# Optimization experiments

Hardware: AMD Instinct MI355X
Metric: run time of the kernel (lower is better)

## Reference

```python
import jax, jax.numpy as jnp
import numpy as np

D_MODEL = 1024
N_HEAD = 16
HEAD_DIM = D_MODEL // N_HEAD
BATCH = 2
SEQ = 2048


def setup_inputs() -> dict:
    key = jax.random.key(0)
    ks = jax.random.split(key, 5)
    std = np.sqrt(2.0 / (D_MODEL + D_MODEL)).astype(np.float32)
    return {
        "in_features": jax.random.normal(ks[0], (BATCH, SEQ, D_MODEL), dtype=jnp.float32),
        "Wq": jax.random.normal(ks[1], (D_MODEL, D_MODEL), dtype=jnp.float32) * std,
        "Wk": jax.random.normal(ks[2], (D_MODEL, D_MODEL), dtype=jnp.float32) * std,
        "Wv": jax.random.normal(ks[3], (D_MODEL, D_MODEL), dtype=jnp.float32) * std,
        "Wo": jax.random.normal(ks[4], (D_MODEL, D_MODEL), dtype=jnp.float32) * std,
    }


def reference(in_features, Wq, Wk, Wv, Wo):
    B, S, _ = in_features.shape
    # projections: x @ W (custom Linear stores weight as [in, out], no bias)
    q = (in_features @ Wq).reshape(B, S, N_HEAD, HEAD_DIM).transpose(0, 2, 1, 3)  # [B,H,S,Dh]
    k = (in_features @ Wk).reshape(B, S, N_HEAD, HEAD_DIM).transpose(0, 2, 1, 3)
    v = (in_features @ Wv).reshape(B, S, N_HEAD, HEAD_DIM).transpose(0, 2, 1, 3)
    scale = HEAD_DIM ** (-0.5)
    scores = jnp.einsum("bhqd,bhkd->bhqk", q, k) * scale  # [B,H,S,S]
    causal = jnp.tril(jnp.ones((S, S), dtype=bool))
    scores = jnp.where(causal, scores, -jnp.inf)
    attn = jax.nn.softmax(scores, axis=-1)
    ctx = jnp.einsum("bhqk,bhkd->bhqd", attn, v)  # [B,H,S,Dh]
    ctx = ctx.transpose(0, 2, 1, 3).reshape(B, S, D_MODEL)
    return ctx @ Wo
```

## Files before the change

kernel.cpp:

```cpp
#include <hip/hip_runtime.h>
#include <hip/hip_bf16.h>

#define DM 1024
#define NH 16
#define HD 64
#define B_ 2
#define S_ 2048
#define M_ (B_*S_)

typedef __attribute__((ext_vector_type(8))) short bf16x8;
typedef __attribute__((ext_vector_type(4))) float f32x4;
typedef __attribute__((ext_vector_type(4))) unsigned uint32x4;
typedef __attribute__((ext_vector_type(2))) unsigned uint32x2;

__device__ __forceinline__ float bf2f(ushort u) {
  union { unsigned u32; float f; } c; c.u32 = ((unsigned)u) << 16; return c.f;
}
__device__ __forceinline__ ushort f2bf(float f) {
  union { float f; unsigned u32; } c; c.f = f;
  unsigned u = c.u32;
  unsigned r = (u + 0x7fffu + ((u >> 16) & 1u)) >> 16;
  return (ushort)r;
}
__device__ __forceinline__ unsigned fbits(float f) {
  union { float f; unsigned u; } c; c.f = f; return c.u;
}

__device__ __forceinline__ void async16(const ushort* g, ushort* l) {
  __builtin_amdgcn_global_load_lds((const __attribute__((address_space(1))) void*)g,
                                   (__attribute__((address_space(3))) void*)l, 16, 0, 0);
}

__device__ __forceinline__ void pswap32(unsigned& a, unsigned& b) {
  uint32x2 r = __builtin_amdgcn_permlane32_swap(a, b, false, false);
  a = r[0]; b = r[1];
}
__device__ __forceinline__ void pswap16(unsigned& a, unsigned& b) {
  uint32x2 r = __builtin_amdgcn_permlane16_swap(a, b, false, false);
  a = r[0]; b = r[1];
}

__global__ void cvt_prep(const float* __restrict__ x, const float* __restrict__ W0,
                         const float* __restrict__ W1, const float* __restrict__ W2,
                         const float* __restrict__ W3, ushort* __restrict__ wt,
                         ushort* __restrict__ xb) {
  __shared__ float tile[64][65];
  int z = blockIdx.z;
  int tx = threadIdx.x, ty = threadIdx.y;
  if (z == 4) {
    int tid = ty * 64 + tx;
    size_t base4 = ((size_t)blockIdx.y * 16 + blockIdx.x) * 4096;
    const float4* xv = (const float4*)x;
    ushort4* ov = (ushort4*)xb;
    #pragma unroll
    for (int k = 0; k < 16; ++k) {
      float4 v = xv[base4 + k * 256 + tid];
      ushort4 o;
      o.x = f2bf(v.x); o.y = f2bf(v.y); o.z = f2bf(v.z); o.w = f2bf(v.w);
      ov[base4 + k * 256 + tid] = o;
    }
    return;
  }
  const float* W = (z == 0) ? W0 : (z == 1) ? W1 : (z == 2) ? W2 : W3;
  ushort* Wt = wt + (size_t)z * (DM * DM);
  int c0 = blockIdx.x * 64, r0 = blockIdx.y * 64;
  #pragma unroll
  for (int i = ty; i < 64; i += 4) tile[i][tx] = W[(size_t)(r0 + i) * DM + c0 + tx];
  __syncthreads();
  #pragma unroll
  for (int i = ty; i < 64; i += 4) Wt[(size_t)(c0 + i) * DM + r0 + tx] = f2bf(tile[tx][i]);
}

template <int MODE, int BN>
__device__ __forceinline__ void gemm_body(const ushort* __restrict__ A,
                                          const ushort* __restrict__ Bt,
                                          ushort* __restrict__ Cb,
                                          float* __restrict__ Cf,
                                          ushort* As, ushort* Bs, ushort* Ts) {
  const int K = DM;
  constexpr int CN = BN / 32;
  int m0 = blockIdx.y * 128;
  int n0 = blockIdx.x * BN;
  int t = threadIdx.x;
  int lane = t & 63, wave = t >> 6;
  int wm = (wave >> 1) * 64, wn = (wave & 1) * (BN / 2);
  int lrow = lane & 15, quad = lane >> 4;

  int Ra = wave * 32;
  int Rb = wave * (BN / 4);
  int srow = lane >> 2, scol = (lane & 3) * 8;

  f32x4 acc[4][CN];
  #pragma unroll
  for (int r = 0; r < 4; ++r)
    #pragma unroll
    for (int c = 0; c < CN; ++c) acc[r][c] = (f32x4){0.f, 0.f, 0.f, 0.f};

  for (int k0 = 0; k0 < K; k0 += 32) {
    const ushort* ga = A + (size_t)(m0 + Ra + srow) * K + k0 + scol;
    const ushort* gb = Bt + (size_t)(n0 + Rb + srow) * K + k0 + scol;
    async16(ga,          As + Ra * 32);
    async16(ga + 16 * K, As + (Ra + 16) * 32);
    async16(gb,          Bs + Rb * 32);
    if (BN == 128) async16(gb + 16 * K, Bs + (Rb + 16) * 32);
    __syncthreads();

    bf16x8 af[4], bfr[CN];
    #pragma unroll
    for (int r = 0; r < 4; ++r)
      af[r] = *(const bf16x8*)(As + (wm + r * 16 + lrow) * 32 + quad * 8);
    #pragma unroll
    for (int c = 0; c < CN; ++c)
      bfr[c] = *(const bf16x8*)(Bs + (wn + c * 16 + lrow) * 32 + quad * 8);
    #pragma unroll
    for (int r = 0; r < 4; ++r)
      #pragma unroll
      for (int c = 0; c < CN; ++c)
        acc[r][c] = __builtin_amdgcn_mfma_f32_16x16x32_bf16(af[r], bfr[c], acc[r][c], 0, 0, 0);
    __syncthreads();
  }

  if constexpr (MODE == 2) {
    int bb = m0 >> 11;
    int s0base = m0 & 2047;
    #pragma unroll
    for (int H = 0; H < 2; ++H) {
      __syncthreads();
      if ((wave >> 1) == H) {
        #pragma unroll
        for (int r = 0; r < 4; ++r)
          #pragma unroll
          for (int c = 0; c < 4; ++c) {
            uint2 pk;
            pk.x = (unsigned)f2bf(acc[r][c][0]) | ((unsigned)f2bf(acc[r][c][1]) << 16);
            pk.y = (unsigned)f2bf(acc[r][c][2]) | ((unsigned)f2bf(acc[r][c][3]) << 16);
            *(uint2*)(Ts + (wn + c * 16 + lrow) * 72 + r * 16 + quad * 4) = pk;
          }
      }
      __syncthreads();
      #pragma unroll
      for (int i = 0; i < 4; ++i) {
        int id = t + i * 256;
        int nn = id >> 3, col = (id & 7) * 8;
        uint4 v = *(const uint4*)(Ts + nn * 72 + col);
        int h2 = (n0 >> 6) + (nn >> 6), d2 = nn & 63;
        size_t dst = (((size_t)(bb * NH + h2)) * HD + d2) * (size_t)S_ + s0base + H * 64 + col;
        *(uint4*)(Cb + dst) = v;
      }
    }
  } else {
    #pragma unroll
    for (int r = 0; r < 4; ++r) {
      #pragma unroll
      for (int c = 0; c < CN; ++c) {
        #pragma unroll
        for (int e = 0; e < 4; ++e) {
          int m = m0 + wm + r * 16 + quad * 4 + e;
          int n = n0 + wn + c * 16 + lrow;
          if (MODE == 0) {
            Cf[(size_t)m * DM + n] = acc[r][c][e];
          } else {
            int b = m >> 11, s = m & 2047, h = n >> 6, d = n & 63;
            Cb[(((size_t)(b * NH + h)) * S_ + s) * HD + d] = f2bf(acc[r][c][e]);
          }
        }
      }
    }
  }
}

__global__ __launch_bounds__(256, 3) void gemm_qkv(const ushort* __restrict__ A,
                                                   const ushort* __restrict__ wt,
                                                   ushort* __restrict__ qkv) {
  __shared__ __align__(16) ushort smem[9216];
  ushort* As = smem;
  ushort* Bs = smem + 4096;
  ushort* Ts = smem;
  int z = blockIdx.z;
  if (z < 2)
    gemm_body<1, 128>(A, wt + (size_t)z * (DM * DM), qkv + (size_t)z * ((size_t)M_ * DM),
                      nullptr, As, Bs, Ts);
  else
    gemm_body<2, 128>(A, wt + (size_t)2 * (DM * DM), qkv + (size_t)2 * ((size_t)M_ * DM),
                      nullptr, As, Bs, Ts);
}

__global__ __launch_bounds__(256, 3) void gemm_out(const ushort* __restrict__ A,
                                                   const ushort* __restrict__ wt,
                                                   float* __restrict__ C) {
  __shared__ __align__(16) ushort As[128 * 32];
  __shared__ __align__(16) ushort Bs[64 * 32];
  gemm_body<0, 64>(A, wt, nullptr, C, As, Bs, nullptr);
}

#define EXPC 0.18033688011f

struct AttnState {
  f32x4 o[4];
  float l;
};

template <bool MASKED>
__device__ __forceinline__ void attn_tile_compute(
    int q0, int kt, bf16x8 qf0, bf16x8 qf1,
    const bf16x8 kf0[4], const bf16x8 kf1[4],
    const bf16x8 vf0[4], const bf16x8 vf1[4],
    AttnState& st, int lrow, int quad) {
  f32x4 s[4];
  __builtin_amdgcn_s_setprio(1);
  #pragma unroll
  for (int c = 0; c < 4; ++c) {
    f32x4 z = (f32x4){0.f, 0.f, 0.f, 0.f};
    z = __builtin_amdgcn_mfma_f32_16x16x32_bf16(kf0[c], qf0, z, 0, 0, 0);
    z = __builtin_amdgcn_mfma_f32_16x16x32_bf16(kf1[c], qf1, z, 0, 0, 0);
    s[c] = z;
  }
  __builtin_amdgcn_s_setprio(0);
  int q = q0 + lrow;
  unsigned w0[4], w1[4];
  #pragma unroll
  for (int c = 0; c < 4; ++c) {
    float pv[4];
    #pragma unroll
    for (int e = 0; e < 4; ++e) {
      float v = __builtin_amdgcn_exp2f(s[c][e] * EXPC);
      if (MASKED) {
        int key = kt + c * 16 + quad * 4 + e;
        v = (key <= q) ? v : 0.f;
      }
      pv[e] = v;
      st.l += v;
    }
    w0[c] = __builtin_amdgcn_perm(fbits(pv[1]), fbits(pv[0]), 0x07060302u);
    w1[c] = __builtin_amdgcn_perm(fbits(pv[3]), fbits(pv[2]), 0x07060302u);
  }

  unsigned a0 = w0[0], b0 = w0[1]; pswap32(a0, b0); pswap16(a0, b0);
  unsigned a1 = w1[0], b1 = w1[1]; pswap32(a1, b1); pswap16(a1, b1);
  unsigned c0 = w0[2], d0 = w0[3]; pswap32(c0, d0); pswap16(c0, d0);
  unsigned c1 = w1[2], d1 = w1[3]; pswap32(c1, d1); pswap16(c1, d1);
  union { uint32x4 u; bf16x8 b; } P0, P1;
  P0.u = (uint32x4){a0, a1, b0, b1};
  P1.u = (uint32x4){c0, c1, d0, d1};

  __builtin_amdgcn_s_setprio(1);
  #pragma unroll
  for (int dt = 0; dt < 4; ++dt) {
    st.o[dt] = __builtin_amdgcn_mfma_f32_16x16x32_bf16(P0.b, vf0[dt], st.o[dt], 0, 0, 0);
    st.o[dt] = __builtin_amdgcn_mfma_f32_16x16x32_bf16(P1.b, vf1[dt], st.o[dt], 0, 0, 0);
  }
  __builtin_amdgcn_s_setprio(0);
}

__global__ __launch_bounds__(256, 2) void attn_mfma(const ushort* __restrict__ Q,
                                                    const ushort* __restrict__ Kmat,
                                                    const ushort* __restrict__ Vt,
                                                    ushort* __restrict__ ctx) {
  __shared__ __align__(16) ushort Ks[2][64 * 72];
  __shared__ __align__(16) ushort Vs[2][64 * 72];
  int t = threadIdx.x;
  int lane = t & 63, wave = t >> 6;
  int lrow = lane & 15, quad = lane >> 4;
  int n = blockIdx.x;
  int qt = 31 - (n >> 5);
  int bh = n & 31;
  const ushort* Kb = Kmat + (size_t)bh * S_ * HD;
  const ushort* Vb = Vt + (size_t)bh * HD * S_;
  int b = bh >> 4, h = bh & 15;

  int r0 = t >> 3, s0 = (t & 7) * 8;
  int r1 = (t + 256) >> 3, s1 = s0;

  int q0 = qt * 64 + wave * 16;
  const ushort* Qp = Q + ((size_t)bh * S_ + q0) * HD;
  bf16x8 qf0 = *(const bf16x8*)(Qp + (size_t)lrow * HD + quad * 8);
  bf16x8 qf1 = *(const bf16x8*)(Qp + (size_t)lrow * HD + 32 + quad * 8);

  AttnState st;
  #pragma unroll
  for (int i = 0; i < 4; ++i) st.o[i] = (f32x4){0.f, 0.f, 0.f, 0.f};
  st.l = 0.f;

  int kend = qt * 64;

  {
    uint4 ka = *(const uint4*)(Kb + (size_t)r0 * HD + s0);
    uint4 kb2 = *(const uint4*)(Kb + (size_t)r1 * HD + s1);
    uint4 va = *(const uint4*)(Vb + (size_t)r0 * S_ + s0);
    uint4 vb2 = *(const uint4*)(Vb + (size_t)r1 * S_ + s1);
    *(uint4*)(Ks[0] + r0 * 72 + s0) = ka;
    *(uint4*)(Ks[0] + r1 * 72 + s1) = kb2;
    *(uint4*)(Vs[0] + r0 * 72 + s0) = va;
    *(uint4*)(Vs[0] + r1 * 72 + s1) = vb2;
  }
  __syncthreads();

  for (int kt = 0; kt <= kend; kt += 64) {
    int cur = (kt >> 6) & 1, nxt = cur ^ 1;
    bool has_next = (kt < kend);

    uint4 ka, kb2, va, vb2;
    if (has_next) {
      int ktn = kt + 64;
      ka  = *(const uint4*)(Kb + (size_t)(ktn + r0) * HD + s0);
      kb2 = *(const uint4*)(Kb + (size_t)(ktn + r1) * HD + s1);
      va  = *(const uint4*)(Vb + (size_t)r0 * S_ + ktn + s0);
      vb2 = *(const uint4*)(Vb + (size_t)r1 * S_ + ktn + s1);
    }

    bf16x8 kf0[4], kf1[4], vf0[4], vf1[4];
    #pragma unroll
    for (int c2 = 0; c2 < 4; ++c2) {
      const ushort* kr = Ks[cur] + (c2 * 16 + lrow) * 72;
      kf0[c2] = *(const bf16x8*)(kr + quad * 8);
      kf1[c2] = *(const bf16x8*)(kr + 32 + quad * 8);
      const ushort* vr = Vs[cur] + (c2 * 16 + lrow) * 72;
      vf0[c2] = *(const bf16x8*)(vr + quad * 8);
      vf1[c2] = *(const bf16x8*)(vr + 32 + quad * 8);
    }

    if (kt < kend)
      attn_tile_compute<false>(q0, kt, qf0, qf1, kf0, kf1, vf0, vf1, st, lrow, quad);
    else
      attn_tile_compute<true>(q0, kt, qf0, qf1, kf0, kf1, vf0, vf1, st, lrow, quad);

    __syncthreads();

    if (has_next) {
      *(uint4*)(Ks[nxt] + r0 * 72 + s0) = ka;
      *(uint4*)(Ks[nxt] + r1 * 72 + s1) = kb2;
      *(uint4*)(Vs[nxt] + r0 * 72 + s0) = va;
      *(uint4*)(Vs[nxt] + r1 * 72 + s1) = vb2;
    }
    __syncthreads();
  }

  {
    float l = st.l;
    l += __shfl_xor(l, 16);
    l += __shfl_xor(l, 32);
    float rl = 1.0f / l;
    #pragma unroll
    for (int e = 0; e < 4; ++e) {
      float rinv = __shfl(rl, quad * 4 + e);
      int q = q0 + quad * 4 + e;
      #pragma unroll
      for (int dt = 0; dt < 4; ++dt)
        ctx[((size_t)b * S_ + q) * DM + h * HD + dt * 16 + lrow] = f2bf(st.o[dt][e] * rinv);
    }
  }
}

extern "C" void kernel_launch(void* const* d_in, const int* in_sizes, int n_in,
                              void* d_out, int out_size, void* d_ws, size_t ws_size,
                              hipStream_t stream) {
  const float* x  = (const float*)d_in[0];
  const float* Wq = (const float*)d_in[1];
  const float* Wk = (const float*)d_in[2];
  const float* Wv = (const float*)d_in[3];
  const float* Wo = (const float*)d_in[4];
  float* out = (float*)d_out;
  ushort* ws = (ushort*)d_ws;

  ushort* xb  = ws;
  ushort* wt  = xb + (size_t)M_ * DM;
  ushort* qkv = wt + (size_t)4 * DM * DM;
  ushort* ctx = qkv + (size_t)3 * M_ * DM;

  cvt_prep<<<dim3(16, 16, 5), dim3(64, 4), 0, stream>>>(x, Wq, Wk, Wv, Wo, wt, xb);
  gemm_qkv<<<dim3(DM / 128, M_ / 128, 3), 256, 0, stream>>>(xb, wt, qkv);
  attn_mfma<<<dim3(32 * B_ * NH), 256, 0, stream>>>(qkv, qkv + (size_t)M_ * DM,
                                                    qkv + (size_t)2 * M_ * DM, ctx);
  gemm_out<<<dim3(DM / 64, M_ / 128), 256, 0, stream>>>(ctx, wt + (size_t)3 * DM * DM, out);
}
```

Measured before the change: 170.2 us.

## Fuse Q, K and V projections into one GEMM kernel sharing the activation tile

The QKV projection GEMM is rewritten so each block loads one 128x32 activation tile and multiplies it against 64-column slices of all three weight matrices. Previously a separate z-slice of the grid handled each projection, so every block reloaded the same activation tile. The fused kernel keeps three accumulator sets, writes Q and K in head-major layout, and transposes V through LDS. It lowers launch bounds to 2 waves per SIMD because of the larger register footprint. Separately, one __syncthreads between tile compute and the next-buffer store in the double-buffered attention loop is removed to cut barrier cost.

Result: no change. 171.3 us (+0.7%).

```diff
diff --git a/kernel.cpp b/kernel.cpp
--- a/kernel.cpp
+++ b/kernel.cpp
@@ -120,9 +120,100 @@
     __syncthreads();
   }
 
-  if constexpr (MODE == 2) {
+  #pragma unroll
+  for (int r = 0; r < 4; ++r) {
+    #pragma unroll
+    for (int c = 0; c < CN; ++c) {
+      #pragma unroll
+      for (int e = 0; e < 4; ++e) {
+        int m = m0 + wm + r * 16 + quad * 4 + e;
+        int n = n0 + wn + c * 16 + lrow;
+        if (MODE == 0) {
+          Cf[(size_t)m * DM + n] = acc[r][c][e];
+        }
+      }
+    }
+  }
+}
+
+__global__ __launch_bounds__(256, 2) void gemm_qkv(const ushort* __restrict__ A,
+                                                   const ushort* __restrict__ wt,
+                                                   ushort* __restrict__ qkv) {
+  __shared__ __align__(16) ushort smem[10240];
+  ushort* As = smem;
+  ushort* Ts = smem;
+  const int K = DM;
+  int m0 = blockIdx.y * 128;
+  int n0 = blockIdx.x * 64;
+  int t = threadIdx.x;
+  int lane = t & 63, wave = t >> 6;
+  int wm = (wave >> 1) * 64, wn = (wave & 1) * 32;
+  int lrow = lane & 15, quad = lane >> 4;
+  int Ra = wave * 32;
+  int Rb = wave * 16;
+  int srow = lane >> 2, scol = (lane & 3) * 8;
+
+  f32x4 acc[3][4][2];
+  #pragma unroll
+  for (int z = 0; z < 3; ++z)
+    #pragma unroll
+    for (int r = 0; r < 4; ++r)
+      #pragma unroll
+      for (int c = 0; c < 2; ++c) acc[z][r][c] = (f32x4){0.f, 0.f, 0.f, 0.f};
+
+  for (int k0 = 0; k0 < K; k0 += 32) {
+    const ushort* ga = A + (size_t)(m0 + Ra + srow) * K + k0 + scol;
+    async16(ga,          As + Ra * 32);
+    async16(ga + 16 * K, As + (Ra + 16) * 32);
+    #pragma unroll
+    for (int z = 0; z < 3; ++z) {
+      const ushort* gb = wt + (size_t)z * (DM * DM) + (size_t)(n0 + Rb + srow) * K + k0 + scol;
+      async16(gb, smem + 4096 + z * 2048 + Rb * 32);
+    }
+    __syncthreads();
+
+    bf16x8 af[4];
+    #pragma unroll
+    for (int r = 0; r < 4; ++r)
+      af[r] = *(const bf16x8*)(As + (wm + r * 16 + lrow) * 32 + quad * 8);
+    #pragma unroll
+    for (int z = 0; z < 3; ++z) {
+      bf16x8 bfr[2];
+      #pragma unroll
+      for (int c = 0; c < 2; ++c)
+        bfr[c] = *(const bf16x8*)(smem + 4096 + z * 2048 + (wn + c * 16 + lrow) * 32 + quad * 8);
+      #pragma unroll
+      for (int r = 0; r < 4; ++r)
+        #pragma unroll
+        for (int c = 0; c < 2; ++c)
+          acc[z][r][c] = __builtin_amdgcn_mfma_f32_16x16x32_bf16(af[r], bfr[c], acc[z][r][c], 0, 0, 0);
+    }
+    __syncthreads();
+  }
+
+  #pragma unroll
+  for (int z = 0; z < 2; ++z) {
+    ushort* Cz = qkv + (size_t)z * ((size_t)M_ * DM);
+    #pragma unroll
+    for (int r = 0; r < 4; ++r) {
+      #pragma unroll
+      for (int c = 0; c < 2; ++c) {
+        #pragma unroll
+        for (int e = 0; e < 4; ++e) {
+          int m = m0 + wm + r * 16 + quad * 4 + e;
+          int n = n0 + wn + c * 16 + lrow;
+          int b = m >> 11, s = m & 2047, h = n >> 6, d = n & 63;
+          Cz[(((size_t)(b * NH + h)) * S_ + s) * HD + d] = f2bf(acc[z][r][c][e]);
+        }
+      }
+    }
+  }
+
+  {
+    ushort* Cb = qkv + (size_t)2 * ((size_t)M_ * DM);
     int bb = m0 >> 11;
     int s0base = m0 & 2047;
+    int h2 = n0 >> 6;
     #pragma unroll
     for (int H = 0; H < 2; ++H) {
       __syncthreads();
@@ -130,59 +221,24 @@
         #pragma unroll
         for (int r = 0; r < 4; ++r)
           #pragma unroll
-          for (int c = 0; c < 4; ++c) {
+          for (int c = 0; c < 2; ++c) {
             uint2 pk;
-            pk.x = (unsigned)f2bf(acc[r][c][0]) | ((unsigned)f2bf(acc[r][c][1]) << 16);
-            pk.y = (unsigned)f2bf(acc[r][c][2]) | ((unsigned)f2bf(acc[r][c][3]) << 16);
+            pk.x = (unsigned)f2bf(acc[2][r][c][0]) | ((unsigned)f2bf(acc[2][r][c][1]) << 16);
+            pk.y = (unsigned)f2bf(acc[2][r][c][2]) | ((unsigned)f2bf(acc[2][r][c][3]) << 16);
             *(uint2*)(Ts + (wn + c * 16 + lrow) * 72 + r * 16 + quad * 4) = pk;
           }
       }
       __syncthreads();
       #pragma unroll
-      for (int i = 0; i < 4; ++i) {
+      for (int i = 0; i < 2; ++i) {
         int id = t + i * 256;
         int nn = id >> 3, col = (id & 7) * 8;
         uint4 v = *(const uint4*)(Ts + nn * 72 + col);
-        int h2 = (n0 >> 6) + (nn >> 6), d2 = nn & 63;
-        size_t dst = (((size_t)(bb * NH + h2)) * HD + d2) * (size_t)S_ + s0base + H * 64 + col;
+        size_t dst = (((size_t)(bb * NH + h2)) * HD + nn) * (size_t)S_ + s0base + H * 64 + col;
         *(uint4*)(Cb + dst) = v;
       }
     }
-  } else {
-    #pragma unroll
-    for (int r = 0; r < 4; ++r) {
-      #pragma unroll
-      for (int c = 0; c < CN; ++c) {
-        #pragma unroll
-        for (int e = 0; e < 4; ++e) {
-          int m = m0 + wm + r * 16 + quad * 4 + e;
-          int n = n0 + wn + c * 16 + lrow;
-          if (MODE == 0) {
-            Cf[(size_t)m * DM + n] = acc[r][c][e];
-          } else {
-            int b = m >> 11, s = m & 2047, h = n >> 6, d = n & 63;
-            Cb[(((size_t)(b * NH + h)) * S_ + s) * HD + d] = f2bf(acc[r][c][e]);
-          }
-        }
-      }
-    }
-  }
-}
-
-__global__ __launch_bounds__(256, 3) void gemm_qkv(const ushort* __restrict__ A,
-                                                   const ushort* __restrict__ wt,
-                                                   ushort* __restrict__ qkv) {
-  __shared__ __align__(16) ushort smem[9216];
-  ushort* As = smem;
-  ushort* Bs = smem + 4096;
-  ushort* Ts = smem;
-  int z = blockIdx.z;
-  if (z < 2)
-    gemm_body<1, 128>(A, wt + (size_t)z * (DM * DM), qkv + (size_t)z * ((size_t)M_ * DM),
-                      nullptr, As, Bs, Ts);
-  else
-    gemm_body<2, 128>(A, wt + (size_t)2 * (DM * DM), qkv + (size_t)2 * ((size_t)M_ * DM),
-                      nullptr, As, Bs, Ts);
+  }
 }
 
 __global__ __launch_bounds__(256, 3) void gemm_out(const ushort* __restrict__ A,
@@ -324,8 +380,6 @@
     else
       attn_tile_compute<true>(q0, kt, qf0, qf1, kf0, kf1, vf0, vf1, st, lrow, quad);
 
-    __syncthreads();
-
     if (has_next) {
       *(uint4*)(Ks[nxt] + r0 * 72 + s0) = ka;
       *(uint4*)(Ks[nxt] + r1 * 72 + s1) = kb2;
@@ -368,7 +422,7 @@
   ushort* ctx = qkv + (size_t)3 * M_ * DM;
 
   cvt_prep<<<dim3(16, 16, 5), dim3(64, 4), 0, stream>>>(x, Wq, Wk, Wv, Wo, wt, xb);
-  gemm_qkv<<<dim3(DM / 128, M_ / 128, 3), 256, 0, stream>>>(xb, wt, qkv);
+  gemm_qkv<<<dim3(DM / 64, M_ / 128), 256, 0, stream>>>(xb, wt, qkv);
   attn_mfma<<<dim3(32 * B_ * NH), 256, 0, stream>>>(qkv, qkv + (size_t)M_ * DM,
                                                     qkv + (size_t)2 * M_ * DM, ctx);
   gemm_out<<<dim3(DM / 64, M_ / 128), 256, 0, stream>>>(ctx, wt + (size_t)3 * DM * DM, out);
```
